# Kernel optimization log

Measured on AMD Instinct MI355X. Metric: run time of the kernel, lower is better.

The kernel has to match this reference:

```python
import jax, jax.numpy as jnp
import numpy as np

B, N, DIM, IN_DIM, H = 8, 3136, 147, 64, 1
HD = IN_DIM // H          # per-head value/key dim = 64
MLP_HID = int(IN_DIM * 1.0)
EPS = 1e-5


def _ln(x, w, b):
    m = jnp.mean(x, axis=-1, keepdims=True)
    v = jnp.mean((x - m) ** 2, axis=-1, keepdims=True)
    return (x - m) / jnp.sqrt(v + EPS) * w + b


def setup_inputs() -> dict:
    key = jax.random.key(0)
    ks = jax.random.split(key, 12)
    r = lambda k, shp, s=0.02: (jax.random.normal(k, shp, dtype=jnp.float32) * s)
    return {
        "x": jax.random.normal(ks[0], (B, N, DIM), dtype=jnp.float32),
        "norm1_w": jnp.ones((DIM,), jnp.float32),
        "norm1_b": jnp.zeros((DIM,), jnp.float32),
        "qkv_w": r(ks[1], (3 * IN_DIM, DIM)),
        "scale": jnp.full((H,), (DIM // H) ** -0.5, dtype=jnp.float32),
        "proj_w": r(ks[2], (IN_DIM, IN_DIM)),
        "proj_b": jnp.zeros((IN_DIM,), jnp.float32),
        "norm2_w": jnp.ones((IN_DIM,), jnp.float32),
        "norm2_b": jnp.zeros((IN_DIM,), jnp.float32),
        "fc1_w": r(ks[3], (MLP_HID, IN_DIM)),
        "fc1_b": jnp.zeros((MLP_HID,), jnp.float32),
        "fc2_w": r(ks[4], (IN_DIM, MLP_HID)),
        "fc2_b": jnp.zeros((IN_DIM,), jnp.float32),
    }


def reference(x, norm1_w, norm1_b, qkv_w, scale, proj_w, proj_b,
              norm2_w, norm2_b, fc1_w, fc1_b, fc2_w, fc2_b):
    h = _ln(x, norm1_w, norm1_b)                               # [B,N,DIM]
    qkv = jnp.einsum('bnc,oc->bno', h, qkv_w)                  # [B,N,3*IN_DIM]
    qkv = qkv.reshape(B, N, 3, H, HD).transpose(2, 0, 3, 1, 4)  # [3,B,H,N,HD]
    q, k, v = qkv[0], qkv[1], qkv[2]
    # LMSA: learnable per-head scale + diagonal (self) exclusion mask
    attn = jnp.einsum('bhid,bhjd->bhij', q, k) * scale[None, :, None, None]
    eye = jnp.eye(N, dtype=bool)
    attn = jnp.where(eye[None, None], -jnp.inf, attn)
    attn = jax.nn.softmax(attn, axis=-1)
    o = jnp.einsum('bhij,bhjd->bhid', attn, v)                 # [B,H,N,HD]
    o = o.transpose(0, 2, 1, 3).reshape(B, N, IN_DIM)
    o = jnp.einsum('bnd,od->bno', o, proj_w) + proj_b
    # num_heads == 1 -> residual is v itself
    x_attn = v[:, 0] + o                                       # [B,N,IN_DIM]
    h2 = _ln(x_attn, norm2_w, norm2_b)
    h2 = jax.nn.gelu(jnp.einsum('bnd,hd->bnh', h2, fc1_w) + fc1_b,
                     approximate=False)
    h2 = jnp.einsum('bnh,oh->bno', h2, fc2_w) + fc2_b
    return x_attn + h2
```

## Files before the change

kernel.cpp:

```cpp
#include <hip/hip_runtime.h>
#include <math.h>

#define B_    8
#define N_    3136
#define DIM_  147
#define KP_   160
#define TOK_  (B_*N_)
#define QKV3_ 192

typedef __attribute__((ext_vector_type(4))) float f32x4;
typedef __attribute__((ext_vector_type(4))) unsigned int u32x4;
typedef __attribute__((ext_vector_type(8))) short short8;
typedef union { short8 s; u32x4 u; } pk8;

static __device__ __forceinline__ unsigned short f2b(float f){
  unsigned int u = __float_as_uint(f);
  u += 0x7fffu + ((u>>16)&1u);
  return (unsigned short)(u>>16);
}
static __device__ __forceinline__ unsigned int pk2(float a, float b){
  return ((unsigned int)f2b(b)<<16) | (unsigned int)f2b(a);
}
static __device__ __forceinline__ unsigned int pk2t(float a, float b){
  return (__float_as_uint(b) & 0xffff0000u) | (__float_as_uint(a)>>16);
}
static __device__ __forceinline__ float b2f(unsigned short s){
  return __uint_as_float(((unsigned int)s)<<16);
}

__global__ __launch_bounds__(256) void k_prep(const float* __restrict__ qkvw,
                                              const float* __restrict__ projw,
                                              const float* __restrict__ fc1w,
                                              const float* __restrict__ fc2w,
                                              unsigned short* __restrict__ wp,
                                              unsigned short* __restrict__ wpj,
                                              unsigned short* __restrict__ w1b,
                                              unsigned short* __restrict__ w2b){
  int idx = blockIdx.x*256 + threadIdx.x;
  if(idx < QKV3_*KP_){
    int n = idx / KP_, k = idx - n*KP_;
    wp[idx] = f2b((k < DIM_) ? qkvw[n*DIM_ + k] : 0.f);
  }
  if(idx < 4096){
    wpj[idx] = f2b(projw[idx]);
    w1b[idx] = f2b(fc1w[idx]);
    w2b[idx] = f2b(fc2w[idx]);
  }
}

__global__ __launch_bounds__(256) void k_qkv(const float* __restrict__ x,
                                             const float* __restrict__ w1,
                                             const float* __restrict__ b1,
                                             const unsigned short* __restrict__ wp,
                                             const float* __restrict__ scale,
                                             unsigned short* __restrict__ qb,
                                             unsigned short* __restrict__ kb,
                                             unsigned short* __restrict__ vtb,
                                             unsigned short* __restrict__ vfb){
  __shared__ alignas(16) float XF[32*147];
  __shared__ alignas(16) unsigned short A_[32*168];
  __shared__ alignas(16) unsigned short VT[64*36];
  int tid = threadIdx.x;
  int w = tid>>6, lane = tid&63, quad = lane>>4, l16 = lane&15;
  int t0 = blockIdx.x*32;
  float sc2 = scale[0] * 1.44269504089f;

  {
    const float* xg = x + (size_t)t0*147;
    for(int i=0;i<19;i++){ int f = i*256 + tid; if(f < 32*147) XF[f] = xg[f]; }
  }
  __syncthreads();
  {
    int g = tid>>3, e = tid&7;
    float s = 0.f, sq = 0.f;
    #pragma unroll
    for(int i=0;i<19;i++){
      int col = e + 8*i;
      float v = (col < 147) ? XF[g*147 + col] : 0.f;
      s += v; sq += v*v;
    }
    s  += __shfl_xor(s,1,64);  s  += __shfl_xor(s,2,64);  s  += __shfl_xor(s,4,64);
    sq += __shfl_xor(sq,1,64); sq += __shfl_xor(sq,2,64); sq += __shfl_xor(sq,4,64);
    float mean = s*(1.f/147.f);
    float var  = sq*(1.f/147.f) - mean*mean;
    float rstd = rsqrtf(var + 1e-5f);
    #pragma unroll
    for(int i=0;i<19;i++){
      int col = e + 8*i;
      if(col < 147) A_[g*168 + col] = f2b((XF[g*147+col]-mean)*rstd*w1[col] + b1[col]);
    }
    #pragma unroll
    for(int i=0;i<2;i++){ int col = 147 + e + 8*i; if(col < 160) A_[g*168 + col] = 0; }
  }
  __syncthreads();
  int mh = (w&1)*16, cb = (w>>1)*96;
  short8 Af[5];
  #pragma unroll
  for(int kk=0;kk<5;kk++)
    Af[kk] = *(const short8*)(A_ + (mh+l16)*168 + kk*32 + quad*8);
  f32x4 acc[6];
  #pragma unroll
  for(int i=0;i<6;i++) acc[i] = (f32x4){0.f,0.f,0.f,0.f};
  #pragma unroll
  for(int nt=0;nt<6;nt++){
    #pragma unroll
    for(int kk=0;kk<5;kk++){
      short8 Bf = *(const short8*)(wp + (size_t)(cb+nt*16+l16)*160 + kk*32 + quad*8);
      acc[nt] = __builtin_amdgcn_mfma_f32_16x16x32_bf16(Af[kk], Bf, acc[nt], 0,0,0);
    }
  }
  #pragma unroll
  for(int nt=0;nt<6;nt++){
    int o = cb + nt*16 + l16;
    #pragma unroll
    for(int r=0;r<4;r++){
      int tl = mh + quad*4 + r;
      int mg = t0 + tl;
      float val = acc[nt][r];
      if(o < 64){
        qb[(size_t)mg*64 + o] = f2b(val*sc2);
      } else if(o < 128){
        kb[(size_t)mg*64 + (o-64)] = f2b(val);
      } else {
        int hd = o - 128;
        unsigned short vb = f2b(val);
        vfb[(size_t)mg*64 + hd] = vb;
        VT[hd*36 + tl] = vb;
      }
    }
  }
  __syncthreads();
  {
    int b = t0 / N_, n0 = t0 - b*N_;
    const unsigned int* VT32 = (const unsigned int*)VT;
    unsigned int* vg = (unsigned int*)vtb + ((size_t)b*64)*(N_/2) + (n0>>1);
    for(int rep=0;rep<4;rep++){
      int f = rep*256 + tid;
      int row = f>>4, c = f&15;
      vg[(size_t)row*(N_/2) + c] = VT32[row*18 + c];
    }
  }
}

__global__ __launch_bounds__(128,4) void k_attn(const unsigned short* __restrict__ qb,
                                                const unsigned short* __restrict__ kb,
                                                const unsigned short* __restrict__ vtb,
                                                unsigned short* __restrict__ Opart,
                                                float* __restrict__ lpart){
  __shared__ alignas(16) unsigned int L[2*64*36];
  unsigned int* Ks = L;
  unsigned int* Vs = L + 64*36;
  int tid = threadIdx.x;
  int w = tid>>6, lane = tid&63, quad = lane>>4, l16 = lane&15;
  int qt = blockIdx.x, sp = blockIdx.y, b = blockIdx.z;
  int kv0 = (sp*49)>>2, kv1 = ((sp+1)*49)>>2;

  short8 Qf[2][2];
  {
    const unsigned short* qg = qb + ((size_t)b*N_ + qt*64 + w*32)*64;
    #pragma unroll
    for(int qs=0;qs<2;qs++)
      #pragma unroll
      for(int kk=0;kk<2;kk++)
        Qf[qs][kk] = *(const short8*)(qg + (qs*16+l16)*64 + kk*32 + quad*8);
  }
  int koff[4], voff[4]; unsigned int ldst_[4];
  const char* kBase = (const char*)kb + (size_t)b*N_*128;
  const char* vBase = (const char*)vtb + (size_t)b*64*(N_*2);
  #pragma unroll
  for(int rr=0;rr<4;rr++){
    int f = rr*128 + tid;
    int p = f>>3, c = f&7;
    int sig = (p&32)|((p&12)<<1)|((p&16)>>2)|(p&3);
    koff[rr] = sig*128 + c*16;
    voff[rr] = p*(N_*2) + c*16;
    ldst_[rr] = p*36 + c*4;
  }
  f32x4 O[2][4];
  #pragma unroll
  for(int qs=0;qs<2;qs++) for(int j=0;j<4;j++) O[qs][j] = (f32x4){0.f,0.f,0.f,0.f};
  float lr[2] = {0.f, 0.f};
  const unsigned short* Ksh = (const unsigned short*)Ks;
  const unsigned short* Vsh = (const unsigned short*)Vs;
  int dloc = w*32 + l16;

  for(int kvt=kv0; kvt<kv1; ++kvt){
    __syncthreads();
    {
      const char* kbB = kBase + (size_t)kvt*8192;
      const char* vbB = vBase + (size_t)kvt*128;
      u32x4 tk[4], tv[4];
      #pragma unroll
      for(int rr=0;rr<4;rr++) tk[rr] = *(const u32x4*)(kbB + koff[rr]);
      #pragma unroll
      for(int rr=0;rr<4;rr++) tv[rr] = *(const u32x4*)(vbB + voff[rr]);
      #pragma unroll
      for(int rr=0;rr<4;rr++) *(u32x4*)&Ks[ldst_[rr]] = tk[rr];
      #pragma unroll
      for(int rr=0;rr<4;rr++) *(u32x4*)&Vs[ldst_[rr]] = tv[rr];
    }
    __syncthreads();

    f32x4 S[2][4];
    f32x4 z = (f32x4){0.f,0.f,0.f,0.f};
    #pragma unroll
    for(int jt=0;jt<4;jt++){
      short8 Kf0 = *(const short8*)(Ksh + (jt*16+l16)*72 + quad*8);
      short8 Kf1 = *(const short8*)(Ksh + (jt*16+l16)*72 + 32 + quad*8);
      S[0][jt] = __builtin_amdgcn_mfma_f32_16x16x32_bf16(Kf0, Qf[0][0], z, 0,0,0);
      S[0][jt] = __builtin_amdgcn_mfma_f32_16x16x32_bf16(Kf1, Qf[0][1], S[0][jt], 0,0,0);
      S[1][jt] = __builtin_amdgcn_mfma_f32_16x16x32_bf16(Kf0, Qf[1][0], z, 0,0,0);
      S[1][jt] = __builtin_amdgcn_mfma_f32_16x16x32_bf16(Kf1, Qf[1][1], S[1][jt], 0,0,0);
    }
    pk8 Pb[2][2];
    if(kvt == qt){
      #pragma unroll
      for(int qs=0;qs<2;qs++){
        int dl = dloc + qs*16;
        float p[4][4];
        #pragma unroll
        for(int jt=0;jt<4;jt++){
          int kvb = (jt>>1)*32 + (jt&1)*4 + quad*8;
          #pragma unroll
          for(int r=0;r<4;r++){
            float pv = (kvb + r == dl) ? 0.f : __builtin_amdgcn_exp2f(S[qs][jt][r]);
            p[jt][r] = pv; lr[qs] += pv;
          }
        }
        Pb[qs][0].u = (u32x4){ pk2t(p[0][0],p[0][1]), pk2t(p[0][2],p[0][3]),
                               pk2t(p[1][0],p[1][1]), pk2t(p[1][2],p[1][3]) };
        Pb[qs][1].u = (u32x4){ pk2t(p[2][0],p[2][1]), pk2t(p[2][2],p[2][3]),
                               pk2t(p[3][0],p[3][1]), pk2t(p[3][2],p[3][3]) };
      }
    } else {
      #pragma unroll
      for(int qs=0;qs<2;qs++){
        float p[4][4];
        #pragma unroll
        for(int jt=0;jt<4;jt++)
          #pragma unroll
          for(int r=0;r<4;r++){
            float pv = __builtin_amdgcn_exp2f(S[qs][jt][r]);
            p[jt][r] = pv; lr[qs] += pv;
          }
        Pb[qs][0].u = (u32x4){ pk2t(p[0][0],p[0][1]), pk2t(p[0][2],p[0][3]),
                               pk2t(p[1][0],p[1][1]), pk2t(p[1][2],p[1][3]) };
        Pb[qs][1].u = (u32x4){ pk2t(p[2][0],p[2][1]), pk2t(p[2][2],p[2][3]),
                               pk2t(p[3][0],p[3][1]), pk2t(p[3][2],p[3][3]) };
      }
    }
    #pragma unroll
    for(int jt2=0;jt2<4;jt2++){
      short8 Vf0 = *(const short8*)(Vsh + (jt2*16+l16)*72 + quad*8);
      short8 Vf1 = *(const short8*)(Vsh + (jt2*16+l16)*72 + 32 + quad*8);
      O[0][jt2] = __builtin_amdgcn_mfma_f32_16x16x32_bf16(Vf0, Pb[0][0].s, O[0][jt2], 0,0,0);
      O[0][jt2] = __builtin_amdgcn_mfma_f32_16x16x32_bf16(Vf1, Pb[0][1].s, O[0][jt2], 0,0,0);
      O[1][jt2] = __builtin_amdgcn_mfma_f32_16x16x32_bf16(Vf0, Pb[1][0].s, O[1][jt2], 0,0,0);
      O[1][jt2] = __builtin_amdgcn_mfma_f32_16x16x32_bf16(Vf1, Pb[1][1].s, O[1][jt2], 0,0,0);
    }
  }
  lr[0] += __shfl_xor(lr[0],16,64); lr[0] += __shfl_xor(lr[0],32,64);
  lr[1] += __shfl_xor(lr[1],16,64); lr[1] += __shfl_xor(lr[1],32,64);
  __syncthreads();
  #pragma unroll
  for(int qs=0;qs<2;qs++){
    int q = w*32 + qs*16 + l16;
    #pragma unroll
    for(int jt2=0;jt2<4;jt2++){
      L[q*36 + jt2*8 + quad*2]     = pk2(O[qs][jt2][0], O[qs][jt2][1]);
      L[q*36 + jt2*8 + quad*2 + 1] = pk2(O[qs][jt2][2], O[qs][jt2][3]);
    }
  }
  if(quad == 0){
    size_t lbase = (size_t)sp*TOK_ + (size_t)b*N_ + qt*64 + w*32;
    lpart[lbase + l16]      = lr[0];
    lpart[lbase + 16 + l16] = lr[1];
  }
  __syncthreads();
  {
    unsigned int* og = (unsigned int*)(Opart + ((size_t)sp*TOK_ + (size_t)b*N_ + qt*64)*64);
    for(int rep=0;rep<4;rep++){
      int f = rep*128 + tid;
      int row = f>>3, c = f&7;
      *(u32x4*)(og + row*32 + c*4) = *(const u32x4*)&L[row*36 + c*4];
    }
  }
}

__global__ __launch_bounds__(128) void k_mlp(const unsigned short* __restrict__ Opart,
                                             const float* __restrict__ lpart,
                                             const unsigned short* __restrict__ vfb,
                                             const unsigned short* __restrict__ wpj,
                                             const unsigned short* __restrict__ w1b,
                                             const unsigned short* __restrict__ w2b,
                                             const float* __restrict__ projb,
                                             const float* __restrict__ n2w,
                                             const float* __restrict__ n2b,
                                             const float* __restrict__ fc1b,
                                             const float* __restrict__ fc2b,
                                             float* __restrict__ out){
  __shared__ alignas(16) unsigned short Xs[32*72];
  unsigned int* Xs32 = (unsigned int*)Xs;
  int tid = threadIdx.x;
  int w = tid>>6, lane = tid&63, quad = lane>>4, l16 = lane&15;
  int t0 = blockIdx.x*32;

  #pragma unroll
  for(int i=0;i<2;i++){
    int f = i*128 + tid;
    int row = f>>3, c = f&7;
    float lo[4] = {0,0,0,0}, hi[4] = {0,0,0,0};
    float lsum = 0.f;
    #pragma unroll
    for(int s=0;s<4;s++){
      u32x4 a = *((const u32x4*)(Opart + ((size_t)s*TOK_ + t0)*64) + row*8 + c);
      #pragma unroll
      for(int k=0;k<4;k++){
        lo[k] += __uint_as_float(a[k]<<16);
        hi[k] += __uint_as_float(a[k] & 0xffff0000u);
      }
      lsum += lpart[(size_t)s*TOK_ + t0 + row];
    }
    float linv = 1.f/lsum;
    u32x4 o;
    #pragma unroll
    for(int k=0;k<4;k++) o[k] = pk2(lo[k]*linv, hi[k]*linv);
    *(u32x4*)&Xs32[row*36 + c*4] = o;
  }
  __syncthreads();

  short8 Af[2];
  #pragma unroll
  for(int kk=0;kk<2;kk++)
    Af[kk] = *(const short8*)(Xs + (w*16+l16)*72 + kk*32 + quad*8);
  f32x4 acc[4];
  #pragma unroll
  for(int i=0;i<4;i++) acc[i] = (f32x4){0.f,0.f,0.f,0.f};
  #pragma unroll
  for(int jt=0;jt<4;jt++)
    #pragma unroll
    for(int kk=0;kk<2;kk++){
      short8 Bf = *(const short8*)(wpj + (jt*16+l16)*64 + kk*32 + quad*8);
      acc[jt] = __builtin_amdgcn_mfma_f32_16x16x32_bf16(Af[kk], Bf, acc[jt], 0,0,0);
    }
  float xa[4][4];
  #pragma unroll
  for(int jt=0;jt<4;jt++){
    int col = jt*16 + l16;
    float pb = projb[col];
    #pragma unroll
    for(int r=0;r<4;r++){
      int tg = t0 + w*16 + quad*4 + r;
      xa[jt][r] = acc[jt][r] + pb + b2f(vfb[(size_t)tg*64 + col]);
    }
  }
  #pragma unroll
  for(int r=0;r<4;r++){
    float s = 0.f, sq = 0.f;
    #pragma unroll
    for(int jt=0;jt<4;jt++){ s += xa[jt][r]; sq += xa[jt][r]*xa[jt][r]; }
    s  += __shfl_xor(s,1,64);  s  += __shfl_xor(s,2,64);
    s  += __shfl_xor(s,4,64);  s  += __shfl_xor(s,8,64);
    sq += __shfl_xor(sq,1,64); sq += __shfl_xor(sq,2,64);
    sq += __shfl_xor(sq,4,64); sq += __shfl_xor(sq,8,64);
    float mu = s*(1.f/64.f);
    float var = sq*(1.f/64.f) - mu*mu;
    float rstd = rsqrtf(var + 1e-5f);
    #pragma unroll
    for(int jt=0;jt<4;jt++){
      int col = jt*16 + l16;
      Xs[(w*16+quad*4+r)*72 + col] = f2b((xa[jt][r]-mu)*rstd*n2w[col] + n2b[col]);
    }
  }
  #pragma unroll
  for(int kk=0;kk<2;kk++)
    Af[kk] = *(const short8*)(Xs + (w*16+l16)*72 + kk*32 + quad*8);
  f32x4 acc2[4];
  #pragma unroll
  for(int i=0;i<4;i++) acc2[i] = (f32x4){0.f,0.f,0.f,0.f};
  #pragma unroll
  for(int jt=0;jt<4;jt++)
    #pragma unroll
    for(int kk=0;kk<2;kk++){
      short8 Bf = *(const short8*)(w1b + (jt*16+l16)*64 + kk*32 + quad*8);
      acc2[jt] = __builtin_amdgcn_mfma_f32_16x16x32_bf16(Af[kk], Bf, acc2[jt], 0,0,0);
    }
  #pragma unroll
  for(int jt=0;jt<4;jt++){
    int col = jt*16 + l16;
    float fb = fc1b[col];
    #pragma unroll
    for(int r=0;r<4;r++){
      float g = acc2[jt][r] + fb;
      float z = g*0.70710678118f;
      float az = fabsf(z);
      float t = 1.f/(1.f + 0.3275911f*az);
      float poly = ((((1.061405429f*t - 1.453152027f)*t + 1.421413741f)*t - 0.284496736f)*t + 0.254829592f)*t;
      float er = 1.f - poly*__builtin_amdgcn_exp2f(-az*az*1.44269504089f);
      er = (z < 0.f) ? -er : er;
      Xs[(w*16+quad*4+r)*72 + col] = f2b(0.5f*g*(1.f + er));
    }
  }
  #pragma unroll
  for(int kk=0;kk<2;kk++)
    Af[kk] = *(const short8*)(Xs + (w*16+l16)*72 + kk*32 + quad*8);
  f32x4 acc3[4];
  #pragma unroll
  for(int i=0;i<4;i++) acc3[i] = (f32x4){0.f,0.f,0.f,0.f};
  #pragma unroll
  for(int jt=0;jt<4;jt++)
    #pragma unroll
    for(int kk=0;kk<2;kk++){
      short8 Bf = *(const short8*)(w2b + (jt*16+l16)*64 + kk*32 + quad*8);
      acc3[jt] = __builtin_amdgcn_mfma_f32_16x16x32_bf16(Af[kk], Bf, acc3[jt], 0,0,0);
    }
  #pragma unroll
  for(int jt=0;jt<4;jt++){
    int col = jt*16 + l16;
    float ob2 = fc2b[col];
    #pragma unroll
    for(int r=0;r<4;r++){
      int tg = t0 + w*16 + quad*4 + r;
      out[(size_t)tg*64 + col] = xa[jt][r] + acc3[jt][r] + ob2;
    }
  }
}

extern "C" void kernel_launch(void* const* d_in, const int* in_sizes, int n_in,
                              void* d_out, int out_size, void* d_ws, size_t ws_size,
                              hipStream_t stream){
  const float* x     = (const float*)d_in[0];
  const float* n1w   = (const float*)d_in[1];
  const float* n1b   = (const float*)d_in[2];
  const float* qkvw  = (const float*)d_in[3];
  const float* scale = (const float*)d_in[4];
  const float* projw = (const float*)d_in[5];
  const float* projb = (const float*)d_in[6];
  const float* n2w   = (const float*)d_in[7];
  const float* n2b   = (const float*)d_in[8];
  const float* fc1w  = (const float*)d_in[9];
  const float* fc1b  = (const float*)d_in[10];
  const float* fc2w  = (const float*)d_in[11];
  const float* fc2b  = (const float*)d_in[12];

  char* base = (char*)d_ws;
  unsigned short* wp  = (unsigned short*)(base + 0);
  unsigned short* wpj = (unsigned short*)(base + 61440);
  unsigned short* w1b = (unsigned short*)(base + 69632);
  unsigned short* w2b = (unsigned short*)(base + 77824);
  unsigned short* qb  = (unsigned short*)(base + 86016);
  unsigned short* kb  = (unsigned short*)(base + 3297280);
  unsigned short* vtb = (unsigned short*)(base + 6508544);
  unsigned short* vfb = (unsigned short*)(base + 9719808);
  unsigned short* Op  = (unsigned short*)(base + 12931072);
  float*          lp  = (float*)(base + 25776128);

  hipLaunchKernelGGL(k_prep, dim3(120),      dim3(256), 0, stream,
                     qkvw, projw, fc1w, fc2w, wp, wpj, w1b, w2b);
  hipLaunchKernelGGL(k_qkv,  dim3(TOK_/32),  dim3(256), 0, stream,
                     x, n1w, n1b, wp, scale, qb, kb, vtb, vfb);
  hipLaunchKernelGGL(k_attn, dim3(49,4,8),   dim3(128), 0, stream, qb, kb, vtb, Op, lp);
  hipLaunchKernelGGL(k_mlp,  dim3(TOK_/32),  dim3(128), 0, stream, Op, lp, vfb,
                     wpj, w1b, w2b, projb, n2w, n2b, fc1b, fc2b, (float*)d_out);
}
```

Before: 150.5 us.

## Load K/V tiles via direct global-to-LDS with XOR swizzle; register-stage LN input

```diff
diff --git a/kernel.cpp b/kernel.cpp
--- a/kernel.cpp
+++ b/kernel.cpp
@@ -1,5 +1,6 @@
 #include <hip/hip_runtime.h>
 #include <math.h>
+#include <stdint.h>
 
 #define B_    8
 #define N_    3136
@@ -27,6 +28,11 @@
 static __device__ __forceinline__ float b2f(unsigned short s){
   return __uint_as_float(((unsigned int)s)<<16);
 }
+
+#define GLD16(gp, lp) __builtin_amdgcn_global_load_lds( \
+    reinterpret_cast<const uint32_t __attribute__((address_space(1)))*>(reinterpret_cast<uintptr_t>(gp)), \
+    reinterpret_cast<uint32_t __attribute__((address_space(3)))*>(reinterpret_cast<uintptr_t>(lp)), \
+    16, 0, 0)
 
 __global__ __launch_bounds__(256) void k_prep(const float* __restrict__ qkvw,
                                               const float* __restrict__ projw,
@@ -48,16 +54,15 @@
   }
 }
 
-__global__ __launch_bounds__(256) void k_qkv(const float* __restrict__ x,
-                                             const float* __restrict__ w1,
-                                             const float* __restrict__ b1,
-                                             const unsigned short* __restrict__ wp,
-                                             const float* __restrict__ scale,
-                                             unsigned short* __restrict__ qb,
-                                             unsigned short* __restrict__ kb,
-                                             unsigned short* __restrict__ vtb,
-                                             unsigned short* __restrict__ vfb){
-  __shared__ alignas(16) float XF[32*147];
+__global__ __launch_bounds__(256,2) void k_qkv(const float* __restrict__ x,
+                                               const float* __restrict__ w1,
+                                               const float* __restrict__ b1,
+                                               const unsigned short* __restrict__ wp,
+                                               const float* __restrict__ scale,
+                                               unsigned short* __restrict__ qb,
+                                               unsigned short* __restrict__ kb,
+                                               unsigned short* __restrict__ vtb,
+                                               unsigned short* __restrict__ vfb){
   __shared__ alignas(16) unsigned short A_[32*168];
   __shared__ alignas(16) unsigned short VT[64*36];
   int tid = threadIdx.x;
@@ -66,18 +71,15 @@
   float sc2 = scale[0] * 1.44269504089f;
 
   {
-    const float* xg = x + (size_t)t0*147;
-    for(int i=0;i<19;i++){ int f = i*256 + tid; if(f < 32*147) XF[f] = xg[f]; }
-  }
-  __syncthreads();
-  {
     int g = tid>>3, e = tid&7;
+    const float* xr = x + (size_t)(t0+g)*147;
+    float xv[19];
     float s = 0.f, sq = 0.f;
     #pragma unroll
     for(int i=0;i<19;i++){
       int col = e + 8*i;
-      float v = (col < 147) ? XF[g*147 + col] : 0.f;
-      s += v; sq += v*v;
+      float v = (col < 147) ? xr[col] : 0.f;
+      xv[i] = v; s += v; sq += v*v;
     }
     s  += __shfl_xor(s,1,64);  s  += __shfl_xor(s,2,64);  s  += __shfl_xor(s,4,64);
     sq += __shfl_xor(sq,1,64); sq += __shfl_xor(sq,2,64); sq += __shfl_xor(sq,4,64);
@@ -87,10 +89,13 @@
     #pragma unroll
     for(int i=0;i<19;i++){
       int col = e + 8*i;
-      if(col < 147) A_[g*168 + col] = f2b((XF[g*147+col]-mean)*rstd*w1[col] + b1[col]);
-    }
-    #pragma unroll
-    for(int i=0;i<2;i++){ int col = 147 + e + 8*i; if(col < 160) A_[g*168 + col] = 0; }
+      if(col < 147) A_[g*168 + col] = f2b((xv[i]-mean)*rstd*w1[col] + b1[col]);
+    }
+    #pragma unroll
+    for(int i=0;i<2;i++){
+      int col = 144 + e + 8*i;
+      if(col >= 147 && col < 160) A_[g*168 + col] = 0;
+    }
   }
   __syncthreads();
   int mh = (w&1)*16, cb = (w>>1)*96;
@@ -147,9 +152,9 @@
                                                 const unsigned short* __restrict__ vtb,
                                                 unsigned short* __restrict__ Opart,
                                                 float* __restrict__ lpart){
-  __shared__ alignas(16) unsigned int L[2*64*36];
+  __shared__ alignas(16) unsigned int L[4096];
   unsigned int* Ks = L;
-  unsigned int* Vs = L + 64*36;
+  unsigned int* Vs = L + 2048;
   int tid = threadIdx.x;
   int w = tid>>6, lane = tid&63, quad = lane>>4, l16 = lane&15;
   int qt = blockIdx.x, sp = blockIdx.y, b = blockIdx.z;
@@ -164,95 +169,87 @@
       for(int kk=0;kk<2;kk++)
         Qf[qs][kk] = *(const short8*)(qg + (qs*16+l16)*64 + kk*32 + quad*8);
   }
-  int koff[4], voff[4]; unsigned int ldst_[4];
+  int koffL[4], voffL[4];
+  {
+    int pl = lane>>3, cl = lane&7;
+    #pragma unroll
+    for(int rr=0;rr<4;rr++){
+      int p = w*32 + rr*8 + pl;
+      int sig = (p&32)|((p&12)<<1)|((p&16)>>2)|(p&3);
+      int cx = cl ^ (p&7);
+      koffL[rr] = sig*128 + cx*16;
+      voffL[rr] = p*(N_*2) + cx*16;
+    }
+  }
   const char* kBase = (const char*)kb + (size_t)b*N_*128;
-  const char* vBase = (const char*)vtb + (size_t)b*64*(N_*2);
-  #pragma unroll
-  for(int rr=0;rr<4;rr++){
-    int f = rr*128 + tid;
-    int p = f>>3, c = f&7;
-    int sig = (p&32)|((p&12)<<1)|((p&16)>>2)|(p&3);
-    koff[rr] = sig*128 + c*16;
-    voff[rr] = p*(N_*2) + c*16;
-    ldst_[rr] = p*36 + c*4;
-  }
+  const char* vBase = (const char*)vtb + (size_t)b*64*(size_t)(N_*2);
+
   f32x4 O[2][4];
   #pragma unroll
   for(int qs=0;qs<2;qs++) for(int j=0;j<4;j++) O[qs][j] = (f32x4){0.f,0.f,0.f,0.f};
   float lr[2] = {0.f, 0.f};
   const unsigned short* Ksh = (const unsigned short*)Ks;
   const unsigned short* Vsh = (const unsigned short*)Vs;
+  int r7 = l16&7;
+  int ku0 = (quad ^ r7)*8;
+  int ku1 = ((4+quad) ^ r7)*8;
   int dloc = w*32 + l16;
 
   for(int kvt=kv0; kvt<kv1; ++kvt){
     __syncthreads();
     {
-      const char* kbB = kBase + (size_t)kvt*8192;
-      const char* vbB = vBase + (size_t)kvt*128;
-      u32x4 tk[4], tv[4];
+      const char* kT = kBase + (size_t)kvt*8192;
+      const char* vT = vBase + (size_t)kvt*128;
       #pragma unroll
-      for(int rr=0;rr<4;rr++) tk[rr] = *(const u32x4*)(kbB + koff[rr]);
+      for(int rr=0;rr<4;rr++){
+        GLD16(kT + koffL[rr], (char*)Ks + (w*32+rr*8)*128);
+        GLD16(vT + voffL[rr], (char*)Vs + (w*32+rr*8)*128);
+      }
+    }
+    __syncthreads();
+
+    pk8 Pb[2][2];
+    #pragma unroll
+    for(int qs=0;qs<2;qs++){
+      f32x4 S[4];
       #pragma unroll
-      for(int rr=0;rr<4;rr++) tv[rr] = *(const u32x4*)(vbB + voff[rr]);
-      #pragma unroll
-      for(int rr=0;rr<4;rr++) *(u32x4*)&Ks[ldst_[rr]] = tk[rr];
-      #pragma unroll
-      for(int rr=0;rr<4;rr++) *(u32x4*)&Vs[ldst_[rr]] = tv[rr];
-    }
-    __syncthreads();
-
-    f32x4 S[2][4];
-    f32x4 z = (f32x4){0.f,0.f,0.f,0.f};
-    #pragma unroll
-    for(int jt=0;jt<4;jt++){
-      short8 Kf0 = *(const short8*)(Ksh + (jt*16+l16)*72 + quad*8);
-      short8 Kf1 = *(const short8*)(Ksh + (jt*16+l16)*72 + 32 + quad*8);
-      S[0][jt] = __builtin_amdgcn_mfma_f32_16x16x32_bf16(Kf0, Qf[0][0], z, 0,0,0);
-      S[0][jt] = __builtin_amdgcn_mfma_f32_16x16x32_bf16(Kf1, Qf[0][1], S[0][jt], 0,0,0);
-      S[1][jt] = __builtin_amdgcn_mfma_f32_16x16x32_bf16(Kf0, Qf[1][0], z, 0,0,0);
-      S[1][jt] = __builtin_amdgcn_mfma_f32_16x16x32_bf16(Kf1, Qf[1][1], S[1][jt], 0,0,0);
-    }
-    pk8 Pb[2][2];
-    if(kvt == qt){
-      #pragma unroll
-      for(int qs=0;qs<2;qs++){
+      for(int jt=0;jt<4;jt++){
+        short8 Kf0 = *(const short8*)(Ksh + jt*1024 + l16*64 + ku0);
+        short8 Kf1 = *(const short8*)(Ksh + jt*1024 + l16*64 + ku1);
+        f32x4 z = (f32x4){0.f,0.f,0.f,0.f};
+        S[jt] = __builtin_amdgcn_mfma_f32_16x16x32_bf16(Kf0, Qf[qs][0], z, 0,0,0);
+        S[jt] = __builtin_amdgcn_mfma_f32_16x16x32_bf16(Kf1, Qf[qs][1], S[jt], 0,0,0);
+      }
+      float p[4][4];
+      if(kvt == qt){
         int dl = dloc + qs*16;
-        float p[4][4];
         #pragma unroll
         for(int jt=0;jt<4;jt++){
           int kvb = (jt>>1)*32 + (jt&1)*4 + quad*8;
           #pragma unroll
           for(int r=0;r<4;r++){
-            float pv = (kvb + r == dl) ? 0.f : __builtin_amdgcn_exp2f(S[qs][jt][r]);
+            float pv = (kvb + r == dl) ? 0.f : __builtin_amdgcn_exp2f(S[jt][r]);
             p[jt][r] = pv; lr[qs] += pv;
           }
         }
-        Pb[qs][0].u = (u32x4){ pk2t(p[0][0],p[0][1]), pk2t(p[0][2],p[0][3]),
-                               pk2t(p[1][0],p[1][1]), pk2t(p[1][2],p[1][3]) };
-        Pb[qs][1].u = (u32x4){ pk2t(p[2][0],p[2][1]), pk2t(p[2][2],p[2][3]),
-                               pk2t(p[3][0],p[3][1]), pk2t(p[3][2],p[3][3]) };
-      }
-    } else {
-      #pragma unroll
-      for(int qs=0;qs<2;qs++){
-        float p[4][4];
+      } else {
         #pragma unroll
         for(int jt=0;jt<4;jt++)
           #pragma unroll
           for(int r=0;r<4;r++){
-            float pv = __builtin_amdgcn_exp2f(S[qs][jt][r]);
+            float pv = __builtin_amdgcn_exp2f(S[jt][r]);
             p[jt][r] = pv; lr[qs] += pv;
           }
-        Pb[qs][0].u = (u32x4){ pk2t(p[0][0],p[0][1]), pk2t(p[0][2],p[0][3]),
-                               pk2t(p[1][0],p[1][1]), pk2t(p[1][2],p[1][3]) };
-        Pb[qs][1].u = (u32x4){ pk2t(p[2][0],p[2][1]), pk2t(p[2][2],p[2][3]),
-                               pk2t(p[3][0],p[3][1]), pk2t(p[3][2],p[3][3]) };
       }
+      Pb[qs][0].u = (u32x4){ pk2t(p[0][0],p[0][1]), pk2t(p[0][2],p[0][3]),
+                             pk2t(p[1][0],p[1][1]), pk2t(p[1][2],p[1][3]) };
+      Pb[qs][1].u = (u32x4){ pk2t(p[2][0],p[2][1]), pk2t(p[2][2],p[2][3]),
+                             pk2t(p[3][0],p[3][1]), pk2t(p[3][2],p[3][3]) };
     }
     #pragma unroll
     for(int jt2=0;jt2<4;jt2++){
-      short8 Vf0 = *(const short8*)(Vsh + (jt2*16+l16)*72 + quad*8);
-      short8 Vf1 = *(const short8*)(Vsh + (jt2*16+l16)*72 + 32 + quad*8);
+      short8 Vf0 = *(const short8*)(Vsh + jt2*1024 + l16*64 + ku0);
+      short8 Vf1 = *(const short8*)(Vsh + jt2*1024 + l16*64 + ku1);
       O[0][jt2] = __builtin_amdgcn_mfma_f32_16x16x32_bf16(Vf0, Pb[0][0].s, O[0][jt2], 0,0,0);
       O[0][jt2] = __builtin_amdgcn_mfma_f32_16x16x32_bf16(Vf1, Pb[0][1].s, O[0][jt2], 0,0,0);
       O[1][jt2] = __builtin_amdgcn_mfma_f32_16x16x32_bf16(Vf0, Pb[1][0].s, O[1][jt2], 0,0,0);
```

Result: slower. 154.2 us (+2.4%).
